# Optimization experiments

Measured on AMD Instinct MI355X. Metric: run time of the kernel, lower is better.

Reference implementation:

```python
import jax, jax.numpy as jnp
import numpy as np

B = 16384
OBJ_FEAT = 1024
PVF_DIM = 1024
PPF_DIM = 64
HIDDEN = 512
OBJ_NUM = 1001        # param['object_num'] + 1
PRED_NUM = 132


def setup_inputs() -> dict:
    key = jax.random.key(0)
    ks = jax.random.split(key, 16)
    s = 0.02
    return {
        "inp_sf":  jax.random.normal(ks[0], (B, OBJ_FEAT), jnp.float32),
        "inp_of":  jax.random.normal(ks[1], (B, OBJ_FEAT), jnp.float32),
        "inp_ppf": jax.random.normal(ks[2], (B, PPF_DIM), jnp.float32),
        "inp_pvf": jax.random.normal(ks[3], (B, PVF_DIM), jnp.float32),
        "gt_s": jax.random.randint(ks[4], (B,), 0, OBJ_NUM, jnp.int32),
        "gt_o": jax.random.randint(ks[5], (B,), 0, OBJ_NUM, jnp.int32),
        # object_predictor: Linear(OBJ_FEAT, HIDDEN) -> Dropout -> ReLU -> Linear(HIDDEN, OBJ_NUM, bias=False)
        "W_obj1": jax.random.normal(ks[6], (OBJ_FEAT, HIDDEN), jnp.float32) * s,
        "b_obj1": jnp.zeros((HIDDEN,), jnp.float32),
        "W_obj2": jax.random.normal(ks[7], (HIDDEN, OBJ_NUM), jnp.float32) * s,
        # predicate_vis_feat_emb: Linear(PVF_DIM, HIDDEN) -> Dropout -> ReLU
        "W_pvf": jax.random.normal(ks[8], (PVF_DIM, HIDDEN), jnp.float32) * s,
        "b_pvf": jnp.zeros((HIDDEN,), jnp.float32),
        # predicate_feat_emb: Linear(HIDDEN + PPF_DIM, HIDDEN) -> ReLU
        "W_pf": jax.random.normal(ks[9], (HIDDEN + PPF_DIM, HIDDEN), jnp.float32) * s,
        "b_pf": jnp.zeros((HIDDEN,), jnp.float32),
        # predicate_predictor: Linear(HIDDEN, PRED_NUM, bias=False)
        "W_pred": jax.random.normal(ks[10], (HIDDEN, PRED_NUM), jnp.float32) * s,
        # knowledge table (frozen) + learnable scalar factor
        "so2p": jax.random.normal(ks[11], (OBJ_NUM * OBJ_NUM, PRED_NUM), jnp.float32) * s,
        "so2p_factor": jnp.zeros((1,), jnp.float32),
    }


def reference(inp_sf, inp_of, inp_ppf, inp_pvf, gt_s, gt_o,
              W_obj1, b_obj1, W_obj2, W_pvf, b_pvf, W_pf, b_pf, W_pred,
              so2p, so2p_factor):
    def obj_predictor(x):
        h = jnp.maximum(x @ W_obj1 + b_obj1, 0.0)  # Dropout is identity (p=0 / eval)
        return h @ W_obj2

    s_score = obj_predictor(inp_sf)               # [B, OBJ_NUM]
    o_score = obj_predictor(inp_of)               # [B, OBJ_NUM]

    pvf_emb = jnp.maximum(inp_pvf @ W_pvf + b_pvf, 0.0)                     # [B, HIDDEN]
    pf_emb = jnp.maximum(jnp.concatenate([pvf_emb, inp_ppf], axis=1) @ W_pf + b_pf, 0.0)
    p_score = pf_emb @ W_pred                     # [B, PRED_NUM]

    # one-hot(s) (x) one-hot(o) flattened then matmul with so2p == row gather at s*OBJ_NUM + o
    so_bias = so2p[gt_s * OBJ_NUM + gt_o]         # [B, PRED_NUM]
    so_bias = so_bias * jnp.exp(so2p_factor)      # use_knowledge=True

    return (s_score, o_score, p_score + so_bias)
```

## Files before the change

### kernel.cpp

```cpp
#include <hip/hip_runtime.h>
#include <hip/hip_bf16.h>
#include <cstdint>
#include <cstddef>

constexpr int BROWS   = 16384;
constexpr int OBJ_FEAT = 1024;
constexpr int PPF_DIM  = 64;
constexpr int HIDDEN   = 512;
constexpr int OBJ_NUM  = 1001;
constexpr int PRED_NUM = 132;
constexpr int OBJ_PAD  = 1024;
constexpr int PRED_PAD = 256;
constexpr int PF_K     = HIDDEN + PPF_DIM;

typedef __attribute__((ext_vector_type(8))) short bf16x8;
typedef __attribute__((ext_vector_type(4))) float f32x4;

static __device__ __forceinline__ unsigned short f2bf(float f) {
  unsigned int u = __float_as_uint(f);
  u += 0x7fffu + ((u >> 16) & 1u);
  return (unsigned short)(u >> 16);
}


__global__ void cast_f32_bf16_vec(const float4* __restrict__ in,
                                  ushort4* __restrict__ out, int n4) {
  int i = blockIdx.x * 256 + threadIdx.x;
  if (i < n4) {
    float4 v = in[i];
    ushort4 o;
    o.x = f2bf(v.x); o.y = f2bf(v.y); o.z = f2bf(v.z); o.w = f2bf(v.w);
    out[i] = o;
  }
}

__global__ void cast_transpose(const float* __restrict__ W,
                               unsigned short* __restrict__ Wt,
                               int K, int N) {
  int k = blockIdx.x * 256 + threadIdx.x;
  int n = blockIdx.y;
  if (k < K) {
    float v = (n < N) ? W[(size_t)k * N + n] : 0.0f;
    Wt[(size_t)n * K + k] = f2bf(v);
  }
}

__global__ void cast_ppf(const float* __restrict__ ppf,
                         unsigned short* __restrict__ Apf) {
  int idx = blockIdx.x * 256 + threadIdx.x;
  int row = idx >> 6, c = idx & 63;
  Apf[(size_t)row * PF_K + HIDDEN + c] = f2bf(ppf[idx]);
}

template <int MODE>
__global__ __launch_bounds__(256)
void gemm_bt(const unsigned short* __restrict__ A,
             const unsigned short* __restrict__ Bt,
             int K,
             float* __restrict__ outF,
             unsigned short* __restrict__ outB,
             int ldout, int Nreal,
             const float* __restrict__ bias,
             const int* __restrict__ gts, const int* __restrict__ gto,
             const float* __restrict__ so2p, const float* __restrict__ factor) {
  __shared__ unsigned short sA[128 * 32];
  __shared__ unsigned short sB[128 * 32];

  const int tid  = threadIdx.x;
  const int lane = tid & 63;
  const int wave = tid >> 6;
  const int wm   = wave >> 1;
  const int wn   = wave & 1;
  const int quad = lane >> 4;
  const int r16  = lane & 15;

  const int m0 = blockIdx.y * 128;
  const int n0 = blockIdx.x * 128;

  f32x4 acc[4][4] = {};

  for (int k0 = 0; k0 < K; k0 += 32) {
    __syncthreads();
#pragma unroll
    for (int j = 0; j < 2; ++j) {
      int chunk = tid + j * 256;
      int row = chunk >> 2;
      int c8  = chunk & 3;
      const unsigned short* ga = A + (size_t)(m0 + row) * K + k0 + c8 * 8;
      __builtin_amdgcn_global_load_lds(
          (const __attribute__((address_space(1))) void*)ga,
          (__attribute__((address_space(3))) void*)(sA + chunk * 8), 16, 0, 0);
      const unsigned short* gb = Bt + (size_t)(n0 + row) * K + k0 + c8 * 8;
      __builtin_amdgcn_global_load_lds(
          (const __attribute__((address_space(1))) void*)gb,
          (__attribute__((address_space(3))) void*)(sB + chunk * 8), 16, 0, 0);
    }
    __syncthreads();

    bf16x8 af[4], bfr[4];
#pragma unroll
    for (int i = 0; i < 4; ++i)
      af[i] = *reinterpret_cast<const bf16x8*>(sA + (wm * 64 + i * 16 + r16) * 32 + quad * 8);
#pragma unroll
    for (int j = 0; j < 4; ++j)
      bfr[j] = *reinterpret_cast<const bf16x8*>(sB + (wn * 64 + j * 16 + r16) * 32 + quad * 8);
#pragma unroll
    for (int i = 0; i < 4; ++i)
#pragma unroll
      for (int j = 0; j < 4; ++j)
        acc[i][j] = __builtin_amdgcn_mfma_f32_16x16x32_bf16(af[i], bfr[j], acc[i][j], 0, 0, 0);
  }

  float ef = 0.0f;
  if (MODE == 2) ef = expf(factor[0]);

#pragma unroll
  for (int i = 0; i < 4; ++i) {
    int mbase = m0 + wm * 64 + i * 16 + quad * 4;
#pragma unroll
    for (int j = 0; j < 4; ++j) {
      int n = n0 + wn * 64 + j * 16 + r16;
      if (n < Nreal) {
#pragma unroll
        for (int reg = 0; reg < 4; ++reg) {
          int m = mbase + reg;
          float v = acc[i][j][reg];
          if (MODE == 0) {
            v = fmaxf(v + bias[n], 0.0f);
            outB[(size_t)m * ldout + n] = f2bf(v);
          } else if (MODE == 1) {
            outF[(size_t)m * ldout + n] = v;
          } else {
            long rowidx = (long)gts[m] * OBJ_NUM + gto[m];
            v += so2p[rowidx * PRED_NUM + n] * ef;
            outF[(size_t)m * ldout + n] = v;
          }
        }
      }
    }
  }
}


extern "C" void kernel_launch(void* const* d_in, const int* in_sizes, int n_in,
                              void* d_out, int out_size, void* d_ws, size_t ws_size,
                              hipStream_t stream) {
  const float* inp_sf  = (const float*)d_in[0];
  const float* inp_of  = (const float*)d_in[1];
  const float* inp_ppf = (const float*)d_in[2];
  const float* inp_pvf = (const float*)d_in[3];
  const int*   gt_s    = (const int*)d_in[4];
  const int*   gt_o    = (const int*)d_in[5];
  const float* W_obj1  = (const float*)d_in[6];
  const float* b_obj1  = (const float*)d_in[7];
  const float* W_obj2  = (const float*)d_in[8];
  const float* W_pvf   = (const float*)d_in[9];
  const float* b_pvf   = (const float*)d_in[10];
  const float* W_pf    = (const float*)d_in[11];
  const float* b_pf    = (const float*)d_in[12];
  const float* W_pred  = (const float*)d_in[13];
  const float* so2p    = (const float*)d_in[14];
  const float* so2p_f  = (const float*)d_in[15];

  float* out_s = (float*)d_out;
  float* out_o = out_s + (size_t)BROWS * OBJ_NUM;
  float* out_p = out_o + (size_t)BROWS * OBJ_NUM;

  char* ws = (char*)d_ws;
  unsigned short* A_buf = (unsigned short*)ws; ws += (size_t)BROWS * 1024 * 2;
  unsigned short* H_buf = (unsigned short*)ws; ws += (size_t)BROWS * 512 * 2;
  unsigned short* Apf   = (unsigned short*)ws; ws += (size_t)BROWS * PF_K * 2;
  unsigned short* Wt_obj1 = (unsigned short*)ws; ws += (size_t)HIDDEN * OBJ_FEAT * 2;
  unsigned short* Wt_obj2 = (unsigned short*)ws; ws += (size_t)OBJ_PAD * HIDDEN * 2;
  unsigned short* Wt_pvf  = (unsigned short*)ws; ws += (size_t)HIDDEN * OBJ_FEAT * 2;
  unsigned short* Wt_pf   = (unsigned short*)ws; ws += (size_t)HIDDEN * PF_K * 2;
  unsigned short* Wt_pred = (unsigned short*)ws; ws += (size_t)PRED_PAD * HIDDEN * 2;

  cast_transpose<<<dim3((OBJ_FEAT + 255) / 256, HIDDEN), 256, 0, stream>>>(W_obj1, Wt_obj1, OBJ_FEAT, HIDDEN);
  cast_transpose<<<dim3((HIDDEN + 255) / 256, OBJ_PAD), 256, 0, stream>>>(W_obj2, Wt_obj2, HIDDEN, OBJ_NUM);
  cast_transpose<<<dim3((OBJ_FEAT + 255) / 256, HIDDEN), 256, 0, stream>>>(W_pvf, Wt_pvf, OBJ_FEAT, HIDDEN);
  cast_transpose<<<dim3((PF_K + 255) / 256, HIDDEN), 256, 0, stream>>>(W_pf, Wt_pf, PF_K, HIDDEN);
  cast_transpose<<<dim3((HIDDEN + 255) / 256, PRED_PAD), 256, 0, stream>>>(W_pred, Wt_pred, HIDDEN, PRED_NUM);

  const int n4_big = BROWS * 1024 / 4;
  const dim3 cgrid((n4_big + 255) / 256);

  cast_f32_bf16_vec<<<cgrid, 256, 0, stream>>>((const float4*)inp_sf, (ushort4*)A_buf, n4_big);
  gemm_bt<0><<<dim3(HIDDEN / 128, BROWS / 128), 256, 0, stream>>>(
      A_buf, Wt_obj1, OBJ_FEAT, nullptr, H_buf, HIDDEN, HIDDEN, b_obj1, nullptr, nullptr, nullptr, nullptr);
  gemm_bt<1><<<dim3(OBJ_PAD / 128, BROWS / 128), 256, 0, stream>>>(
      H_buf, Wt_obj2, HIDDEN, out_s, nullptr, OBJ_NUM, OBJ_NUM, nullptr, nullptr, nullptr, nullptr, nullptr);

  cast_f32_bf16_vec<<<cgrid, 256, 0, stream>>>((const float4*)inp_of, (ushort4*)A_buf, n4_big);
  gemm_bt<0><<<dim3(HIDDEN / 128, BROWS / 128), 256, 0, stream>>>(
      A_buf, Wt_obj1, OBJ_FEAT, nullptr, H_buf, HIDDEN, HIDDEN, b_obj1, nullptr, nullptr, nullptr, nullptr);
  gemm_bt<1><<<dim3(OBJ_PAD / 128, BROWS / 128), 256, 0, stream>>>(
      H_buf, Wt_obj2, HIDDEN, out_o, nullptr, OBJ_NUM, OBJ_NUM, nullptr, nullptr, nullptr, nullptr, nullptr);

  cast_f32_bf16_vec<<<cgrid, 256, 0, stream>>>((const float4*)inp_pvf, (ushort4*)A_buf, n4_big);
  cast_ppf<<<dim3(BROWS * PPF_DIM / 256), 256, 0, stream>>>(inp_ppf, Apf);
  gemm_bt<0><<<dim3(HIDDEN / 128, BROWS / 128), 256, 0, stream>>>(
      A_buf, Wt_pvf, OBJ_FEAT, nullptr, Apf, PF_K, HIDDEN, b_pvf, nullptr, nullptr, nullptr, nullptr);
  gemm_bt<0><<<dim3(HIDDEN / 128, BROWS / 128), 256, 0, stream>>>(
      Apf, Wt_pf, PF_K, nullptr, H_buf, HIDDEN, HIDDEN, b_pf, nullptr, nullptr, nullptr, nullptr);
  gemm_bt<2><<<dim3(PRED_PAD / 128, BROWS / 128), 256, 0, stream>>>(
      H_buf, Wt_pred, HIDDEN, out_p, nullptr, PRED_NUM, PRED_NUM, nullptr, gt_s, gt_o, so2p, so2p_f);

  (void)in_sizes; (void)n_in; (void)out_size; (void)ws_size;
}
```

Before: 996.1 us.

## Fuse input casts into GEMM A-load and batch subject/object paths

```diff
diff --git a/kernel.cpp b/kernel.cpp
--- a/kernel.cpp
+++ b/kernel.cpp
@@ -22,47 +22,37 @@
   return (unsigned short)(u >> 16);
 }
 
-
-__global__ void cast_f32_bf16_vec(const float4* __restrict__ in,
-                                  ushort4* __restrict__ out, int n4) {
-  int i = blockIdx.x * 256 + threadIdx.x;
-  if (i < n4) {
-    float4 v = in[i];
-    ushort4 o;
-    o.x = f2bf(v.x); o.y = f2bf(v.y); o.z = f2bf(v.z); o.w = f2bf(v.w);
-    out[i] = o;
-  }
-}
-
-__global__ void cast_transpose(const float* __restrict__ W,
-                               unsigned short* __restrict__ Wt,
-                               int K, int N) {
+__global__ void cast_w_all(const float* __restrict__ W0, const float* __restrict__ W1,
+                           const float* __restrict__ W2, const float* __restrict__ W3,
+                           const float* __restrict__ W4,
+                           unsigned short* __restrict__ T0, unsigned short* __restrict__ T1,
+                           unsigned short* __restrict__ T2, unsigned short* __restrict__ T3,
+                           unsigned short* __restrict__ T4) {
+  const int z = blockIdx.z;
+  const float* W; unsigned short* T; int K, N, Npad;
+  if      (z == 0) { W = W0; T = T0; K = 1024; N = 512;  Npad = 512;  }
+  else if (z == 1) { W = W1; T = T1; K = 512;  N = 1001; Npad = 1024; }
+  else if (z == 2) { W = W2; T = T2; K = 1024; N = 512;  Npad = 512;  }
+  else if (z == 3) { W = W3; T = T3; K = 576;  N = 512;  Npad = 512;  }
+  else             { W = W4; T = T4; K = 512;  N = 132;  Npad = 256;  }
+  int n = blockIdx.y;
   int k = blockIdx.x * 256 + threadIdx.x;
-  int n = blockIdx.y;
-  if (k < K) {
-    float v = (n < N) ? W[(size_t)k * N + n] : 0.0f;
-    Wt[(size_t)n * K + k] = f2bf(v);
-  }
-}
-
-__global__ void cast_ppf(const float* __restrict__ ppf,
-                         unsigned short* __restrict__ Apf) {
-  int idx = blockIdx.x * 256 + threadIdx.x;
-  int row = idx >> 6, c = idx & 63;
-  Apf[(size_t)row * PF_K + HIDDEN + c] = f2bf(ppf[idx]);
+  if (n >= Npad || k >= K) return;
+  float v = (n < N) ? W[(size_t)k * N + n] : 0.0f;
+  T[(size_t)n * K + k] = f2bf(v);
 }
 
 template <int MODE>
 __global__ __launch_bounds__(256)
-void gemm_bt(const unsigned short* __restrict__ A,
-             const unsigned short* __restrict__ Bt,
-             int K,
-             float* __restrict__ outF,
-             unsigned short* __restrict__ outB,
-             int ldout, int Nreal,
-             const float* __restrict__ bias,
-             const int* __restrict__ gts, const int* __restrict__ gto,
-             const float* __restrict__ so2p, const float* __restrict__ factor) {
+void gemm_fused(const unsigned short* __restrict__ Ab, int ldAb, int K1,
+                const float* __restrict__ Af0, const float* __restrict__ Af1,
+                int M1f, int ldAf,
+                const unsigned short* __restrict__ Bt, int K,
+                float* __restrict__ outF, unsigned short* __restrict__ outB,
+                int ldout, int Nreal,
+                const float* __restrict__ bias,
+                const int* __restrict__ gts, const int* __restrict__ gto,
+                const float* __restrict__ so2p, const float* __restrict__ factor) {
   __shared__ unsigned short sA[128 * 32];
   __shared__ unsigned short sB[128 * 32];
 
@@ -73,29 +63,60 @@
   const int wn   = wave & 1;
   const int quad = lane >> 4;
   const int r16  = lane & 15;
-
-  const int m0 = blockIdx.y * 128;
-  const int n0 = blockIdx.x * 128;
+  const int m0   = blockIdx.y * 128;
+  const int n0   = blockIdx.x * 128;
+
+  const float* afb = nullptr;
+  if (K1 < K)
+    afb = (m0 < M1f) ? (Af0 + (size_t)m0 * ldAf)
+                     : (Af1 + (size_t)(m0 - M1f) * ldAf);
+
+  float4 pa[4];
+  auto loadA = [&](int k0) {
+    const int kf = k0 - K1;
+#pragma unroll
+    for (int j = 0; j < 4; ++j) {
+      int ch = tid + j * 256, row = ch >> 3, c4 = (ch & 7) * 4;
+      pa[j] = *reinterpret_cast<const float4*>(afb + (size_t)row * ldAf + kf + c4);
+    }
+  };
+  if (K1 == 0 && K1 < K) loadA(0);
 
   f32x4 acc[4][4] = {};
 
   for (int k0 = 0; k0 < K; k0 += 32) {
     __syncthreads();
+    if (k0 < K1) {
+#pragma unroll
+      for (int j = 0; j < 2; ++j) {
+        int ch = tid + j * 256, row = ch >> 2, c8 = ch & 3;
+        const unsigned short* ga = Ab + (size_t)(m0 + row) * ldAb + k0 + c8 * 8;
+        __builtin_amdgcn_global_load_lds(
+            (const __attribute__((address_space(1))) void*)ga,
+            (__attribute__((address_space(3))) void*)(sA + ch * 8), 16, 0, 0);
+      }
+    } else {
+#pragma unroll
+      for (int j = 0; j < 4; ++j) {
+        int ch = tid + j * 256, row = ch >> 3, c4 = (ch & 7) * 4;
+        ushort4 o;
+        o.x = f2bf(pa[j].x); o.y = f2bf(pa[j].y);
+        o.z = f2bf(pa[j].z); o.w = f2bf(pa[j].w);
+        *reinterpret_cast<ushort4*>(sA + row * 32 + c4) = o;
+      }
+    }
 #pragma unroll
     for (int j = 0; j < 2; ++j) {
-      int chunk = tid + j * 256;
-      int row = chunk >> 2;
-      int c8  = chunk & 3;
-      const unsigned short* ga = A + (size_t)(m0 + row) * K + k0 + c8 * 8;
-      __builtin_amdgcn_global_load_lds(
-          (const __attribute__((address_space(1))) void*)ga,
-          (__attribute__((address_space(3))) void*)(sA + chunk * 8), 16, 0, 0);
+      int ch = tid + j * 256, row = ch >> 2, c8 = ch & 3;
       const unsigned short* gb = Bt + (size_t)(n0 + row) * K + k0 + c8 * 8;
       __builtin_amdgcn_global_load_lds(
           (const __attribute__((address_space(1))) void*)gb,
-          (__attribute__((address_space(3))) void*)(sB + chunk * 8), 16, 0, 0);
+          (__attribute__((address_space(3))) void*)(sB + ch * 8), 16, 0, 0);
     }
     __syncthreads();
+
+    int kn = k0 + 32;
+    if (kn >= K1 && kn < K) loadA(kn);
 
     bf16x8 af[4], bfr[4];
 #pragma unroll
@@ -163,48 +184,45 @@
   const float* so2p_f  = (const float*)d_in[15];
 
   float* out_s = (float*)d_out;
-  float* out_o = out_s + (size_t)BROWS * OBJ_NUM;
-  float* out_p = out_o + (size_t)BROWS * OBJ_NUM;
+  float* out_p = out_s + 2 * (size_t)BROWS * OBJ_NUM;
 
   char* ws = (char*)d_ws;
-  unsigned short* A_buf = (unsigned short*)ws; ws += (size_t)BROWS * 1024 * 2;
-  unsigned short* H_buf = (unsigned short*)ws; ws += (size_t)BROWS * 512 * 2;
-  unsigned short* Apf   = (unsigned short*)ws; ws += (size_t)BROWS * PF_K * 2;
+  unsigned short* H_buf = (unsigned short*)ws; ws += (size_t)2 * BROWS * HIDDEN * 2;
+  unsigned short* H2    = (unsigned short*)ws; ws += (size_t)BROWS * HIDDEN * 2;
   unsigned short* Wt_obj1 = (unsigned short*)ws; ws += (size_t)HIDDEN * OBJ_FEAT * 2;
   unsigned short* Wt_obj2 = (unsigned short*)ws; ws += (size_t)OBJ_PAD * HIDDEN * 2;
   unsigned short* Wt_pvf  = (unsigned short*)ws; ws += (size_t)HIDDEN * OBJ_FEAT * 2;
   unsigned short* Wt_pf   = (unsigned short*)ws; ws += (size_t)HIDDEN * PF_K * 2;
   unsigned short* Wt_pred = (unsigned short*)ws; ws += (size_t)PRED_PAD * HIDDEN * 2;
 
-  cast_transpose<<<dim3((OBJ_FEAT + 255) / 256, HIDDEN), 256, 0, stream>>>(W_obj1, Wt_obj1, OBJ_FEAT, HIDDEN);
-  cast_transpose<<<dim3((HIDDEN + 255) / 256, OBJ_PAD), 256, 0, stream>>>(W_obj2, Wt_obj2, HIDDEN, OBJ_NUM);
-  cast_transpose<<<dim3((OBJ_FEAT + 255) / 256, HIDDEN), 256, 0, stream>>>(W_pvf, Wt_pvf, OBJ_FEAT, HIDDEN);
-  cast_transpose<<<dim3((PF_K + 255) / 256, HIDDEN), 256, 0, stream>>>(W_pf, Wt_pf, PF_K, HIDDEN);
-  cast_transpose<<<dim3((HIDDEN + 255) / 256, PRED_PAD), 256, 0, stream>>>(W_pred, Wt_pred, HIDDEN, PRED_NUM);
-
-  const int n4_big = BROWS * 1024 / 4;
-  const dim3 cgrid((n4_big + 255) / 256);
-
-  cast_f32_bf16_vec<<<cgrid, 256, 0, stream>>>((const float4*)inp_sf, (ushort4*)A_buf, n4_big);
-  gemm_bt<0><<<dim3(HIDDEN / 128, BROWS / 128), 256, 0, stream>>>(
-      A_buf, Wt_obj1, OBJ_FEAT, nullptr, H_buf, HIDDEN, HIDDEN, b_obj1, nullptr, nullptr, nullptr, nullptr);
-  gemm_bt<1><<<dim3(OBJ_PAD / 128, BROWS / 128), 256, 0, stream>>>(
-      H_buf, Wt_obj2, HIDDEN, out_s, nullptr, OBJ_NUM, OBJ_NUM, nullptr, nullptr, nullptr, nullptr, nullptr);
-
-  cast_f32_bf16_vec<<<cgrid, 256, 0, stream>>>((const float4*)inp_of, (ushort4*)A_buf, n4_big);
-  gemm_bt<0><<<dim3(HIDDEN / 128, BROWS / 128), 256, 0, stream>>>(
-      A_buf, Wt_obj1, OBJ_FEAT, nullptr, H_buf, HIDDEN, HIDDEN, b_obj1, nullptr, nullptr, nullptr, nullptr);
-  gemm_bt<1><<<dim3(OBJ_PAD / 128, BROWS / 128), 256, 0, stream>>>(
-      H_buf, Wt_obj2, HIDDEN, out_o, nullptr, OBJ_NUM, OBJ_NUM, nullptr, nullptr, nullptr, nullptr, nullptr);
-
-  cast_f32_bf16_vec<<<cgrid, 256, 0, stream>>>((const float4*)inp_pvf, (ushort4*)A_buf, n4_big);
-  cast_ppf<<<dim3(BROWS * PPF_DIM / 256), 256, 0, stream>>>(inp_ppf, Apf);
-  gemm_bt<0><<<dim3(HIDDEN / 128, BROWS / 128), 256, 0, stream>>>(
-      A_buf, Wt_pvf, OBJ_FEAT, nullptr, Apf, PF_K, HIDDEN, b_pvf, nullptr, nullptr, nullptr, nullptr);
-  gemm_bt<0><<<dim3(HIDDEN / 128, BROWS / 128), 256, 0, stream>>>(
-      Apf, Wt_pf, PF_K, nullptr, H_buf, HIDDEN, HIDDEN, b_pf, nullptr, nullptr, nullptr, nullptr);
-  gemm_bt<2><<<dim3(PRED_PAD / 128, BROWS / 128), 256, 0, stream>>>(
-      H_buf, Wt_pred, HIDDEN, out_p, nullptr, PRED_NUM, PRED_NUM, nullptr, gt_s, gt_o, so2p, so2p_f);
+  cast_w_all<<<dim3(4, 1024, 5), 256, 0, stream>>>(
+      W_obj1, W_obj2, W_pvf, W_pf, W_pred,
+      Wt_obj1, Wt_obj2, Wt_pvf, Wt_pf, Wt_pred);
+
+  gemm_fused<0><<<dim3(HIDDEN / 128, 2 * BROWS / 128), 256, 0, stream>>>(
+      nullptr, 0, 0, inp_sf, inp_of, BROWS, OBJ_FEAT,
+      Wt_obj1, OBJ_FEAT, nullptr, H_buf, HIDDEN, HIDDEN, b_obj1,
+      nullptr, nullptr, nullptr, nullptr);
+
+  gemm_fused<1><<<dim3(OBJ_PAD / 128, 2 * BROWS / 128), 256, 0, stream>>>(
+      H_buf, HIDDEN, HIDDEN, nullptr, nullptr, 0, 0,
+      Wt_obj2, HIDDEN, out_s, nullptr, OBJ_NUM, OBJ_NUM, nullptr,
+      nullptr, nullptr, nullptr, nullptr);
+
+  gemm_fused<0><<<dim3(HIDDEN / 128, BROWS / 128), 256, 0, stream>>>(
+      nullptr, 0, 0, inp_pvf, inp_pvf, 1 << 30, OBJ_FEAT,
+      Wt_pvf, OBJ_FEAT, nullptr, H_buf, HIDDEN, HIDDEN, b_pvf,
+      nullptr, nullptr, nullptr, nullptr);
+
+  gemm_fused<0><<<dim3(HIDDEN / 128, BROWS / 128), 256, 0, stream>>>(
+      H_buf, HIDDEN, HIDDEN, inp_ppf, inp_ppf, 1 << 30, PPF_DIM,
+      Wt_pf, PF_K, nullptr, H2, HIDDEN, HIDDEN, b_pf,
+      nullptr, nullptr, nullptr, nullptr);
+
+  gemm_fused<2><<<dim3(PRED_PAD / 128, BROWS / 128), 256, 0, stream>>>(
+      H2, HIDDEN, HIDDEN, nullptr, nullptr, 0, 0,
+      Wt_pred, HIDDEN, out_p, nullptr, PRED_NUM, PRED_NUM, nullptr,
+      gt_s, gt_o, so2p, so2p_f);
 
   (void)in_sizes; (void)n_in; (void)out_size; (void)ws_size;
 }
```

Result: no change. 996.1 us (-0.0%).
